# Optimization experiments

Measured on AMD Instinct MI355X. Metric: run time of the kernel, lower is better.

Reference implementation:

```python
import jax, jax.numpy as jnp
import numpy as np

B, S, E, H, D = 4, 2048, 1024, 16, 64

def setup_inputs() -> dict:
    key = jax.random.key(0)
    ks = jax.random.split(key, 9)
    sc = 0.02
    return {
        "x":  jax.random.normal(ks[0], (B, S, E), jnp.float32),
        "Wq": jax.random.normal(ks[1], (H, E, D), jnp.float32) * sc,
        "bq": jax.random.normal(ks[2], (H, D), jnp.float32) * sc,
        "Wk": jax.random.normal(ks[3], (H, E, D), jnp.float32) * sc,
        "bk": jax.random.normal(ks[4], (H, D), jnp.float32) * sc,
        "Wv": jax.random.normal(ks[5], (H, E, D), jnp.float32) * sc,
        "bv": jax.random.normal(ks[6], (H, D), jnp.float32) * sc,
        "Wp": jax.random.normal(ks[7], (H * D, E), jnp.float32) * sc,
        "bp": jax.random.normal(ks[8], (E,), jnp.float32) * sc,
    }

def reference(x, Wq, bq, Wk, bk, Wv, bv, Wp, bp):
    # Per-head projections (stacked): [B,S,E] x [H,E,D] -> [B,H,S,D]
    q = jnp.einsum('bse,hed->bhsd', x, Wq) + bq[None, :, None, :]
    k = jnp.einsum('bse,hed->bhsd', x, Wk) + bk[None, :, None, :]
    v = jnp.einsum('bse,hed->bhsd', x, Wv) + bv[None, :, None, :]
    # Scaled scores with causal mask: [B,H,S,S]
    scores = jnp.einsum('bhqd,bhkd->bhqk', q, k) / jnp.sqrt(jnp.float32(D))
    causal = jnp.tril(jnp.ones((S, S), dtype=bool))
    scores = jnp.where(causal[None, None], scores, -jnp.inf)
    attn = jax.nn.softmax(scores, axis=-1)
    out = jnp.einsum('bhqk,bhkd->bhqd', attn, v)          # [B,H,S,D]
    out = out.transpose(0, 2, 1, 3).reshape(B, S, H * D)  # concat heads
    return out @ Wp + bp                                   # [B,S,E]
```

## Files before the change

kernel.cpp:

```cpp
#include <hip/hip_runtime.h>
#include <hip/hip_bf16.h>

#define B_ 4
#define S_ 2048
#define E_ 1024
#define H_ 16
#define D_ 64
#define QSCALE 0.18033688011112042f

typedef __attribute__((ext_vector_type(8))) short bf16x8;
typedef __attribute__((ext_vector_type(4))) float f32x4;

__device__ __forceinline__ f32x4 mfma16(bf16x8 a, bf16x8 b, f32x4 c) {
    return __builtin_amdgcn_mfma_f32_16x16x32_bf16(a, b, c, 0, 0, 0);
}
__device__ __forceinline__ short f2bs(float f) {
    __hip_bfloat16 h = __float2bfloat16(f);
    return *reinterpret_cast<short*>(&h);
}

__global__ __launch_bounds__(256) void conv_wqkv(
    const float* __restrict__ Wq, const float* __restrict__ Wk,
    const float* __restrict__ Wv, short* __restrict__ WT)
{
    const int mat = blockIdx.x >> 4;
    const int kt  = blockIdx.x & 15;
    const int which = mat >> 4, h = mat & 15;
    const float* src = (which == 0 ? Wq : which == 1 ? Wk : Wv) + (size_t)h * E_ * D_;
    __shared__ float T[64][65];
    const int tid = threadIdx.x;
    const int k0 = kt * 64;
    #pragma unroll
    for (int it = 0; it < 4; ++it) {
        int lin = tid + it * 256;
        int kr = lin >> 4, dc = (lin & 15) * 4;
        const float4 v = *(const float4*)&src[(size_t)(k0 + kr) * D_ + dc];
        T[kr][dc] = v.x; T[kr][dc + 1] = v.y; T[kr][dc + 2] = v.z; T[kr][dc + 3] = v.w;
    }
    __syncthreads();
    #pragma unroll
    for (int it = 0; it < 4; ++it) {
        int lin = tid + it * 256;
        int dr = lin >> 4, kc = (lin & 15) * 4;
        ushort4 o;
        o.x = (unsigned short)f2bs(T[kc][dr]);
        o.y = (unsigned short)f2bs(T[kc + 1][dr]);
        o.z = (unsigned short)f2bs(T[kc + 2][dr]);
        o.w = (unsigned short)f2bs(T[kc + 3][dr]);
        *(ushort4*)&WT[((size_t)mat * 64 + dr) * E_ + k0 + kc] = o;
    }
}

__global__ __launch_bounds__(256) void conv_wp(
    const float* __restrict__ Wp, short* __restrict__ WpT)
{
    const int ktile = blockIdx.x & 15, ntile = blockIdx.x >> 4;
    const int k0 = ktile * 64, n0 = ntile * 64;
    __shared__ float T[64][65];
    const int tid = threadIdx.x;
    #pragma unroll
    for (int it = 0; it < 4; ++it) {
        int lin = tid + it * 256;
        int kr = lin >> 4, nc = (lin & 15) * 4;
        const float4 v = *(const float4*)&Wp[(size_t)(k0 + kr) * E_ + n0 + nc];
        T[kr][nc] = v.x; T[kr][nc + 1] = v.y; T[kr][nc + 2] = v.z; T[kr][nc + 3] = v.w;
    }
    __syncthreads();
    #pragma unroll
    for (int it = 0; it < 4; ++it) {
        int lin = tid + it * 256;
        int nr = lin >> 4, kc = (lin & 15) * 4;
        ushort4 o;
        o.x = (unsigned short)f2bs(T[kc][nr]);
        o.y = (unsigned short)f2bs(T[kc + 1][nr]);
        o.z = (unsigned short)f2bs(T[kc + 2][nr]);
        o.w = (unsigned short)f2bs(T[kc + 3][nr]);
        *(ushort4*)&WpT[(size_t)(n0 + nr) * E_ + k0 + kc] = o;
    }
}

__global__ __launch_bounds__(256, 2) void qkv_fused(
    const float* __restrict__ x, const short* __restrict__ WT,
    const float* __restrict__ bq, const float* __restrict__ bk,
    const float* __restrict__ bv,
    short* __restrict__ Qw, short* __restrict__ Kw, short* __restrict__ VTw)
{
    const int h = blockIdx.y;
    const int m0 = blockIdx.x * 128;
    __shared__ short Xs[128 * 72];
    __shared__ short Wt3[3][64 * 72];

    const int tid = threadIdx.x;
    const int lane = tid & 63, w = tid >> 6;
    const int l15 = lane & 15, qd = lane >> 4;

    f32x4 zero = {0.f, 0.f, 0.f, 0.f};
    f32x4 acc[3][2][4];
    #pragma unroll
    for (int a = 0; a < 3; ++a)
        #pragma unroll
        for (int b = 0; b < 2; ++b)
            #pragma unroll
            for (int c = 0; c < 4; ++c) acc[a][b][c] = zero;

    float4 xr[4][2];
    bf16x8 wr[6];

    #pragma unroll
    for (int it = 0; it < 4; ++it) {
        int lin = tid + it * 256;
        int row = lin >> 3, cb = (lin & 7) * 8;
        xr[it][0] = *(const float4*)&x[(size_t)(m0 + row) * E_ + cb];
        xr[it][1] = *(const float4*)&x[(size_t)(m0 + row) * E_ + cb + 4];
    }
    #pragma unroll
    for (int it = 0; it < 6; ++it) {
        int lin = tid + it * 256;
        int mat = lin >> 9, rem = lin & 511;
        int d = rem >> 3, cb = (rem & 7) * 8;
        wr[it] = *(const bf16x8*)&WT[((size_t)(mat * 16 + h) * 64 + d) * E_ + cb];
    }

    for (int k0 = 0; k0 < E_; k0 += 64) {
        #pragma unroll
        for (int it = 0; it < 4; ++it) {
            int lin = tid + it * 256;
            int row = lin >> 3, cb = (lin & 7) * 8;
            bf16x8 pk;
            pk[0] = f2bs(xr[it][0].x); pk[1] = f2bs(xr[it][0].y);
            pk[2] = f2bs(xr[it][0].z); pk[3] = f2bs(xr[it][0].w);
            pk[4] = f2bs(xr[it][1].x); pk[5] = f2bs(xr[it][1].y);
            pk[6] = f2bs(xr[it][1].z); pk[7] = f2bs(xr[it][1].w);
            *(bf16x8*)&Xs[row * 72 + cb] = pk;
        }
        #pragma unroll
        for (int it = 0; it < 6; ++it) {
            int lin = tid + it * 256;
            int mat = lin >> 9, rem = lin & 511;
            int d = rem >> 3, cb = (rem & 7) * 8;
            *(bf16x8*)&Wt3[mat][d * 72 + cb] = wr[it];
        }
        __syncthreads();
        if (k0 + 64 < E_) {
            #pragma unroll
            for (int it = 0; it < 4; ++it) {
                int lin = tid + it * 256;
                int row = lin >> 3, cb = (lin & 7) * 8;
                xr[it][0] = *(const float4*)&x[(size_t)(m0 + row) * E_ + k0 + 64 + cb];
                xr[it][1] = *(const float4*)&x[(size_t)(m0 + row) * E_ + k0 + 64 + cb + 4];
            }
            #pragma unroll
            for (int it = 0; it < 6; ++it) {
                int lin = tid + it * 256;
                int mat = lin >> 9, rem = lin & 511;
                int d = rem >> 3, cb = (rem & 7) * 8;
                wr[it] = *(const bf16x8*)&WT[((size_t)(mat * 16 + h) * 64 + d) * E_ + k0 + 64 + cb];
            }
        }
        #pragma unroll
        for (int t = 0; t < 2; ++t) {
            bf16x8 am0 = *(const bf16x8*)&Xs[(w * 32 + l15) * 72 + t * 32 + qd * 8];
            bf16x8 am1 = *(const bf16x8*)&Xs[(w * 32 + 16 + l15) * 72 + t * 32 + qd * 8];
            #pragma unroll
            for (int mat = 0; mat < 3; ++mat)
                #pragma unroll
                for (int c = 0; c < 4; ++c) {
                    bf16x8 bb = *(const bf16x8*)&Wt3[mat][(c * 16 + l15) * 72 + t * 32 + qd * 8];
                    acc[mat][0][c] = mfma16(am0, bb, acc[mat][0][c]);
                    acc[mat][1][c] = mfma16(am1, bb, acc[mat][1][c]);
                }
        }
        __syncthreads();
    }

    const int bb = m0 >> 11;
    const int s0 = m0 & (S_ - 1);
    float bqv[4], bkv[4], bvv[4];
    #pragma unroll
    for (int c = 0; c < 4; ++c) {
        int d = c * 16 + l15;
        bqv[c] = bq[h * D_ + d];
        bkv[c] = bk[h * D_ + d];
        bvv[c] = bv[h * D_ + d];
    }
    #pragma unroll
    for (int mi = 0; mi < 2; ++mi)
        #pragma unroll
        for (int c = 0; c < 4; ++c)
            #pragma unroll
            for (int r = 0; r < 4; ++r) {
                int s = s0 + w * 32 + mi * 16 + qd * 4 + r;
                size_t base = (((size_t)bb * H_ + h) * S_ + s) * D_ + c * 16 + l15;
                Qw[base] = f2bs((acc[0][mi][c][r] + bqv[c]) * QSCALE);
                Kw[base] = f2bs(acc[1][mi][c][r] + bkv[c]);
            }
    short* ep = Xs + w * (32 * 66);
    #pragma unroll
    for (int mi = 0; mi < 2; ++mi)
        #pragma unroll
        for (int c = 0; c < 4; ++c)
            #pragma unroll
            for (int r = 0; r < 4; ++r)
                ep[(mi * 16 + qd * 4 + r) * 66 + c * 16 + l15] =
                    f2bs(acc[2][mi][c][r] + bvv[c]);
    asm volatile("s_waitcnt lgkmcnt(0)" ::: "memory");
    const int sr = lane & 31, dh = lane >> 5;
    const size_t vbase = ((size_t)bb * H_ + h) * (size_t)D_ * S_;
    #pragma unroll
    for (int it = 0; it < 32; ++it) {
        int dd = it * 2 + dh;
        VTw[vbase + (size_t)dd * S_ + s0 + w * 32 + sr] = ep[sr * 66 + dd];
    }
}

__global__ __launch_bounds__(256, 2) void attn(
    const short* __restrict__ Qw, const short* __restrict__ Kw,
    const short* __restrict__ VTw, short* __restrict__ Ow)
{
    const int jj = blockIdx.x;
    const int bh = blockIdx.y;
    const int b = bh >> 4, h = bh & 15;
    const size_t kbase = ((size_t)b * H_ + h) * (size_t)S_ * D_;
    const size_t vbase = ((size_t)b * H_ + h) * (size_t)D_ * S_;

    __shared__ short Qs[128 * 72];
    __shared__ short Ks[2][64 * 72];
    __shared__ short Vt[2][64 * 72];

    const int tid = threadIdx.x;
    const int lane = tid & 63, w = tid >> 6;
    const int l15 = lane & 15, qd = lane >> 4;

    const int r0s = tid >> 3;
    const int c0s = (tid & 7) * 8;
    const int r1s = r0s + 32;

    #pragma unroll
    for (int phase = 0; phase < 2; ++phase) {
        const int qt = phase ? jj : (15 - jj);

        #pragma unroll
        for (int it = 0; it < 4; ++it) {
            int row = w * 32 + it * 8 + (lane >> 3);
            int cb = (lane & 7) * 8;
            *(bf16x8*)&Qs[row * 72 + cb] =
                *(const bf16x8*)&Qw[kbase + (size_t)(qt * 128 + row) * D_ + cb];
        }
        asm volatile("s_waitcnt lgkmcnt(0)" ::: "memory");
        bf16x8 qf[2][2];
        #pragma unroll
        for (int mi = 0; mi < 2; ++mi)
            #pragma unroll
            for (int t = 0; t < 2; ++t)
                qf[mi][t] = *(const bf16x8*)&Qs[(w * 32 + mi * 16 + l15) * 72 + t * 32 + qd * 8];

        f32x4 zero = {0.f, 0.f, 0.f, 0.f};
        f32x4 oacc[2][4];
        float lrow[2][4];
        #pragma unroll
        for (int mi = 0; mi < 2; ++mi) {
            #pragma unroll
            for (int c = 0; c < 4; ++c) oacc[mi][c] = zero;
            #pragma unroll
            for (int r = 0; r < 4; ++r) lrow[mi][r] = 0.f;
        }

        const int nkt = (qt + 1) * 2;
        bf16x8 kr0, kr1, vr0, vr1;
        kr0 = *(const bf16x8*)&Kw[kbase + (size_t)r0s * D_ + c0s];
        kr1 = *(const bf16x8*)&Kw[kbase + (size_t)r1s * D_ + c0s];
        vr0 = *(const bf16x8*)&VTw[vbase + (size_t)r0s * S_ + c0s];
        vr1 = *(const bf16x8*)&VTw[vbase + (size_t)r1s * S_ + c0s];
        *(bf16x8*)&Ks[0][r0s * 72 + c0s] = kr0;
        *(bf16x8*)&Ks[0][r1s * 72 + c0s] = kr1;
        *(bf16x8*)&Vt[0][r0s * 72 + c0s] = vr0;
        *(bf16x8*)&Vt[0][r1s * 72 + c0s] = vr1;
        __syncthreads();

        int p = 0;
        for (int kt = 0; kt < nkt; ++kt) {
            const bool pre = (kt + 1 < nkt);
            if (pre) {
                kr0 = *(const bf16x8*)&Kw[kbase + (size_t)((kt + 1) * 64 + r0s) * D_ + c0s];
                kr1 = *(const bf16x8*)&Kw[kbase + (size_t)((kt + 1) * 64 + r1s) * D_ + c0s];
                vr0 = *(const bf16x8*)&VTw[vbase + (size_t)r0s * S_ + (kt + 1) * 64 + c0s];
                vr1 = *(const bf16x8*)&VTw[vbase + (size_t)r1s * S_ + (kt + 1) * 64 + c0s];
            }
            f32x4 sc[2][4];
            #pragma unroll
            for (int mi = 0; mi < 2; ++mi)
                #pragma unroll
                for (int c = 0; c < 4; ++c) sc[mi][c] = zero;
            #pragma unroll
            for (int t = 0; t < 2; ++t)
                #pragma unroll
                for (int c = 0; c < 4; ++c) {
                    bf16x8 bk = *(const bf16x8*)&Ks[p][(c * 16 + l15) * 72 + t * 32 + qd * 8];
                    sc[0][c] = mfma16(qf[0][t], bk, sc[0][c]);
                    sc[1][c] = mfma16(qf[1][t], bk, sc[1][c]);
                }
            #pragma unroll
            for (int mi = 0; mi < 2; ++mi) {
                const int fr = qt * 128 + w * 32 + mi * 16;
                if (kt * 64 + 63 > fr) {
                    #pragma unroll
                    for (int c = 0; c < 4; ++c) {
                        int col = kt * 64 + c * 16 + l15;
                        #pragma unroll
                        for (int r = 0; r < 4; ++r)
                            if (col > fr + qd * 4 + r) sc[mi][c][r] = -1e30f;
                    }
                }
                #pragma unroll
                for (int c = 0; c < 4; ++c)
                    #pragma unroll
                    for (int r = 0; r < 4; ++r) {
                        float pv = __builtin_amdgcn_exp2f(sc[mi][c][r]);
                        lrow[mi][r] += pv;
                        Qs[(w * 32 + mi * 16 + qd * 4 + r) * 72 + c * 16 + l15] = f2bs(pv);
                    }
            }
            asm volatile("s_waitcnt lgkmcnt(0)" ::: "memory");
            #pragma unroll
            for (int t = 0; t < 2; ++t) {
                bf16x8 ap0 = *(const bf16x8*)&Qs[(w * 32 + l15) * 72 + t * 32 + qd * 8];
                bf16x8 ap1 = *(const bf16x8*)&Qs[(w * 32 + 16 + l15) * 72 + t * 32 + qd * 8];
                #pragma unroll
                for (int c = 0; c < 4; ++c) {
                    bf16x8 bv = *(const bf16x8*)&Vt[p][(c * 16 + l15) * 72 + t * 32 + qd * 8];
                    oacc[0][c] = mfma16(ap0, bv, oacc[0][c]);
                    oacc[1][c] = mfma16(ap1, bv, oacc[1][c]);
                }
            }
            if (pre) {
                *(bf16x8*)&Ks[1 - p][r0s * 72 + c0s] = kr0;
                *(bf16x8*)&Ks[1 - p][r1s * 72 + c0s] = kr1;
                *(bf16x8*)&Vt[1 - p][r0s * 72 + c0s] = vr0;
                *(bf16x8*)&Vt[1 - p][r1s * 72 + c0s] = vr1;
            }
            __syncthreads();
            p ^= 1;
        }

        #pragma unroll
        for (int mi = 0; mi < 2; ++mi) {
            float inv[4];
            #pragma unroll
            for (int r = 0; r < 4; ++r) {
                float l = lrow[mi][r];
                l += __shfl_xor(l, 1);
                l += __shfl_xor(l, 2);
                l += __shfl_xor(l, 4);
                l += __shfl_xor(l, 8);
                inv[r] = 1.f / l;
            }
            #pragma unroll
            for (int c = 0; c < 4; ++c)
                #pragma unroll
                for (int r = 0; r < 4; ++r) {
                    int s = qt * 128 + w * 32 + mi * 16 + qd * 4 + r;
                    Ow[((size_t)b * S_ + s) * (H_ * D_) + h * D_ + c * 16 + l15] =
                        f2bs(oacc[mi][c][r] * inv[r]);
                }
        }
    }
}

__global__ __launch_bounds__(256, 3) void out_proj(
    const short* __restrict__ Oin, const short* __restrict__ WpT,
    const float* __restrict__ bp, float* __restrict__ out)
{
    const int m0 = blockIdx.x * 128;
    const int n0 = blockIdx.y * 64;
    __shared__ short As[128 * 72];
    __shared__ short Bs[64 * 72];
    const int tid = threadIdx.x;
    const int lane = tid & 63, w = tid >> 6;
    const int l15 = lane & 15, qd = lane >> 4;

    f32x4 zero = {0.f, 0.f, 0.f, 0.f};
    f32x4 acc[2][4];
    #pragma unroll
    for (int mi = 0; mi < 2; ++mi)
        #pragma unroll
        for (int c = 0; c < 4; ++c) acc[mi][c] = zero;

    bf16x8 ar[4], br[2];
    #pragma unroll
    for (int it = 0; it < 4; ++it) {
        int lin = tid + it * 256;
        int row = lin >> 3, cb = (lin & 7) * 8;
        ar[it] = *(const bf16x8*)&Oin[(size_t)(m0 + row) * E_ + cb];
    }
    #pragma unroll
    for (int it = 0; it < 2; ++it) {
        int lin = tid + it * 256;
        int row = lin >> 3, cb = (lin & 7) * 8;
        br[it] = *(const bf16x8*)&WpT[(size_t)(n0 + row) * E_ + cb];
    }

    for (int k0 = 0; k0 < E_; k0 += 64) {
        #pragma unroll
        for (int it = 0; it < 4; ++it) {
            int lin = tid + it * 256;
            int row = lin >> 3, cb = (lin & 7) * 8;
            *(bf16x8*)&As[row * 72 + cb] = ar[it];
        }
        #pragma unroll
        for (int it = 0; it < 2; ++it) {
            int lin = tid + it * 256;
            int row = lin >> 3, cb = (lin & 7) * 8;
            *(bf16x8*)&Bs[row * 72 + cb] = br[it];
        }
        __syncthreads();
        if (k0 + 64 < E_) {
            #pragma unroll
            for (int it = 0; it < 4; ++it) {
                int lin = tid + it * 256;
                int row = lin >> 3, cb = (lin & 7) * 8;
                ar[it] = *(const bf16x8*)&Oin[(size_t)(m0 + row) * E_ + k0 + 64 + cb];
            }
            #pragma unroll
            for (int it = 0; it < 2; ++it) {
                int lin = tid + it * 256;
                int row = lin >> 3, cb = (lin & 7) * 8;
                br[it] = *(const bf16x8*)&WpT[(size_t)(n0 + row) * E_ + k0 + 64 + cb];
            }
        }
        #pragma unroll
        for (int t = 0; t < 2; ++t) {
            bf16x8 a0 = *(const bf16x8*)&As[(w * 32 + l15) * 72 + t * 32 + qd * 8];
            bf16x8 a1 = *(const bf16x8*)&As[(w * 32 + 16 + l15) * 72 + t * 32 + qd * 8];
            #pragma unroll
            for (int c = 0; c < 4; ++c) {
                bf16x8 bb = *(const bf16x8*)&Bs[(c * 16 + l15) * 72 + t * 32 + qd * 8];
                acc[0][c] = mfma16(a0, bb, acc[0][c]);
                acc[1][c] = mfma16(a1, bb, acc[1][c]);
            }
        }
        __syncthreads();
    }
    #pragma unroll
    for (int mi = 0; mi < 2; ++mi)
        #pragma unroll
        for (int c = 0; c < 4; ++c) {
            float bpv = bp[n0 + c * 16 + l15];
            #pragma unroll
            for (int r = 0; r < 4; ++r) {
                int m = m0 + w * 32 + mi * 16 + qd * 4 + r;
                out[(size_t)m * E_ + n0 + c * 16 + l15] = acc[mi][c][r] + bpv;
            }
        }
}

extern "C" void kernel_launch(void* const* d_in, const int* in_sizes, int n_in,
                              void* d_out, int out_size, void* d_ws, size_t ws_size,
                              hipStream_t stream)
{
    const float* x  = (const float*)d_in[0];
    const float* Wq = (const float*)d_in[1];
    const float* bq = (const float*)d_in[2];
    const float* Wk = (const float*)d_in[3];
    const float* bk = (const float*)d_in[4];
    const float* Wv = (const float*)d_in[5];
    const float* bv = (const float*)d_in[6];
    const float* Wp = (const float*)d_in[7];
    const float* bp = (const float*)d_in[8];
    float* out = (float*)d_out;

    const size_t nQKV = (size_t)B_ * H_ * S_ * D_;
    short* Qw   = (short*)d_ws;
    short* Kw   = Qw + nQKV;
    short* VTw  = Kw + nQKV;
    short* buf3 = VTw + nQKV;
    short* WT   = buf3;
    short* Ow   = buf3;
    short* WpT  = Qw;

    conv_wqkv<<<dim3(768), 256, 0, stream>>>(Wq, Wk, Wv, WT);
    qkv_fused<<<dim3(64, 16), 256, 0, stream>>>(x, WT, bq, bk, bv, Qw, Kw, VTw);
    attn<<<dim3(8, 64), 256, 0, stream>>>(Qw, Kw, VTw, Ow);
    conv_wp<<<dim3(256), 256, 0, stream>>>(Wp, WpT);
    out_proj<<<dim3(64, 16), 256, 0, stream>>>(Ow, WpT, bp, out);
}
```

Baseline: 261.4 us.

## Switch QKV and output projections to 32x32 MFMA with k-slab LDS layout

Both projection GEMMs now use 32x32x16 bf16 MFMA with a 2x2 wave grid instead of 16x16x32 tiles, and shared memory is reorganized into per-k-chunk slabs (padded strides) to cut LDS read traffic and bank conflicts. The output projection tile grows to 128x128 (grid halved), raising arithmetic intensity but lowering occupancy. The V transpose epilogue now goes through a shared buffer with 16-byte vectorized global stores. Register pressure rises from the larger f32x16 accumulators.

Result: faster. 252.3 us (-3.5%).

```diff
diff --git a/kernel.cpp b/kernel.cpp
--- a/kernel.cpp
+++ b/kernel.cpp
@@ -10,14 +10,21 @@
 
 typedef __attribute__((ext_vector_type(8))) short bf16x8;
 typedef __attribute__((ext_vector_type(4))) float f32x4;
+typedef __attribute__((ext_vector_type(16))) float f32x16;
 
 __device__ __forceinline__ f32x4 mfma16(bf16x8 a, bf16x8 b, f32x4 c) {
     return __builtin_amdgcn_mfma_f32_16x16x32_bf16(a, b, c, 0, 0, 0);
+}
+__device__ __forceinline__ f32x16 mfma32(bf16x8 a, bf16x8 b, f32x16 c) {
+    return __builtin_amdgcn_mfma_f32_32x32x16_bf16(a, b, c, 0, 0, 0);
 }
 __device__ __forceinline__ short f2bs(float f) {
     __hip_bfloat16 h = __float2bfloat16(f);
     return *reinterpret_cast<short*>(&h);
 }
+
+#define XSLAB 1032
+#define WSLAB 1544
 
 __global__ __launch_bounds__(256) void conv_wqkv(
     const float* __restrict__ Wq, const float* __restrict__ Wk,
@@ -87,129 +94,128 @@
 {
     const int h = blockIdx.y;
     const int m0 = blockIdx.x * 128;
-    __shared__ short Xs[128 * 72];
-    __shared__ short Wt3[3][64 * 72];
+    __shared__ short SM[8 * XSLAB + 8 * WSLAB];
+    short* Xs = SM;
+    short* Ws = SM + 8 * XSLAB;
 
     const int tid = threadIdx.x;
     const int lane = tid & 63, w = tid >> 6;
-    const int l15 = lane & 15, qd = lane >> 4;
-
-    f32x4 zero = {0.f, 0.f, 0.f, 0.f};
-    f32x4 acc[3][2][4];
-    #pragma unroll
-    for (int a = 0; a < 3; ++a)
-        #pragma unroll
-        for (int b = 0; b < 2; ++b)
-            #pragma unroll
-            for (int c = 0; c < 4; ++c) acc[a][b][c] = zero;
+    const int wm = w & 1, wn = w >> 1;
+    const int l31 = lane & 31, hi = lane >> 5;
+    const int cc = tid & 7, r8 = tid >> 3;
+
+    f32x16 acc[2][3];
+    #pragma unroll
+    for (int mf = 0; mf < 2; ++mf)
+        #pragma unroll
+        for (int nf = 0; nf < 3; ++nf)
+            #pragma unroll
+            for (int i = 0; i < 16; ++i) acc[mf][nf][i] = 0.f;
 
     float4 xr[4][2];
     bf16x8 wr[6];
 
     #pragma unroll
     for (int it = 0; it < 4; ++it) {
-        int lin = tid + it * 256;
-        int row = lin >> 3, cb = (lin & 7) * 8;
-        xr[it][0] = *(const float4*)&x[(size_t)(m0 + row) * E_ + cb];
-        xr[it][1] = *(const float4*)&x[(size_t)(m0 + row) * E_ + cb + 4];
+        const float* p = &x[(size_t)(m0 + it * 32 + r8) * E_ + cc * 8];
+        xr[it][0] = *(const float4*)p;
+        xr[it][1] = *(const float4*)(p + 4);
     }
     #pragma unroll
     for (int it = 0; it < 6; ++it) {
-        int lin = tid + it * 256;
-        int mat = lin >> 9, rem = lin & 511;
-        int d = rem >> 3, cb = (rem & 7) * 8;
-        wr[it] = *(const bf16x8*)&WT[((size_t)(mat * 16 + h) * 64 + d) * E_ + cb];
+        int rg = ((it >> 1) * 16 + h) * 64 + (it & 1) * 32 + r8;
+        wr[it] = *(const bf16x8*)&WT[(size_t)rg * E_ + cc * 8];
     }
 
     for (int k0 = 0; k0 < E_; k0 += 64) {
         #pragma unroll
         for (int it = 0; it < 4; ++it) {
-            int lin = tid + it * 256;
-            int row = lin >> 3, cb = (lin & 7) * 8;
             bf16x8 pk;
             pk[0] = f2bs(xr[it][0].x); pk[1] = f2bs(xr[it][0].y);
             pk[2] = f2bs(xr[it][0].z); pk[3] = f2bs(xr[it][0].w);
             pk[4] = f2bs(xr[it][1].x); pk[5] = f2bs(xr[it][1].y);
             pk[6] = f2bs(xr[it][1].z); pk[7] = f2bs(xr[it][1].w);
-            *(bf16x8*)&Xs[row * 72 + cb] = pk;
-        }
-        #pragma unroll
-        for (int it = 0; it < 6; ++it) {
-            int lin = tid + it * 256;
-            int mat = lin >> 9, rem = lin & 511;
-            int d = rem >> 3, cb = (rem & 7) * 8;
-            *(bf16x8*)&Wt3[mat][d * 72 + cb] = wr[it];
-        }
+            *(bf16x8*)&Xs[cc * XSLAB + (it * 32 + r8) * 8] = pk;
+        }
+        #pragma unroll
+        for (int it = 0; it < 6; ++it)
+            *(bf16x8*)&Ws[cc * WSLAB + (it * 32 + r8) * 8] = wr[it];
         __syncthreads();
         if (k0 + 64 < E_) {
             #pragma unroll
             for (int it = 0; it < 4; ++it) {
-                int lin = tid + it * 256;
-                int row = lin >> 3, cb = (lin & 7) * 8;
-                xr[it][0] = *(const float4*)&x[(size_t)(m0 + row) * E_ + k0 + 64 + cb];
-                xr[it][1] = *(const float4*)&x[(size_t)(m0 + row) * E_ + k0 + 64 + cb + 4];
+                const float* p = &x[(size_t)(m0 + it * 32 + r8) * E_ + k0 + 64 + cc * 8];
+                xr[it][0] = *(const float4*)p;
+                xr[it][1] = *(const float4*)(p + 4);
             }
             #pragma unroll
             for (int it = 0; it < 6; ++it) {
-                int lin = tid + it * 256;
-                int mat = lin >> 9, rem = lin & 511;
-                int d = rem >> 3, cb = (rem & 7) * 8;
-                wr[it] = *(const bf16x8*)&WT[((size_t)(mat * 16 + h) * 64 + d) * E_ + k0 + 64 + cb];
-            }
-        }
-        #pragma unroll
-        for (int t = 0; t < 2; ++t) {
-            bf16x8 am0 = *(const bf16x8*)&Xs[(w * 32 + l15) * 72 + t * 32 + qd * 8];
-            bf16x8 am1 = *(const bf16x8*)&Xs[(w * 32 + 16 + l15) * 72 + t * 32 + qd * 8];
-            #pragma unroll
-            for (int mat = 0; mat < 3; ++mat)
-                #pragma unroll
-                for (int c = 0; c < 4; ++c) {
-                    bf16x8 bb = *(const bf16x8*)&Wt3[mat][(c * 16 + l15) * 72 + t * 32 + qd * 8];
-                    acc[mat][0][c] = mfma16(am0, bb, acc[mat][0][c]);
-                    acc[mat][1][c] = mfma16(am1, bb, acc[mat][1][c]);
-                }
+                int rg = ((it >> 1) * 16 + h) * 64 + (it & 1) * 32 + r8;
+                wr[it] = *(const bf16x8*)&WT[(size_t)rg * E_ + k0 + 64 + cc * 8];
+            }
+        }
+        #pragma unroll
+        for (int ks = 0; ks < 4; ++ks) {
+            const int ccr = ks * 2 + hi;
+            bf16x8 a[2], b[3];
+            #pragma unroll
+            for (int mf = 0; mf < 2; ++mf)
+                a[mf] = *(const bf16x8*)&Xs[ccr * XSLAB + (wm * 64 + mf * 32 + l31) * 8];
+            #pragma unroll
+            for (int nf = 0; nf < 3; ++nf)
+                b[nf] = *(const bf16x8*)&Ws[ccr * WSLAB + (wn * 96 + nf * 32 + l31) * 8];
+            #pragma unroll
+            for (int mf = 0; mf < 2; ++mf)
+                #pragma unroll
+                for (int nf = 0; nf < 3; ++nf)
+                    acc[mf][nf] = mfma32(a[mf], b[nf], acc[mf][nf]);
         }
         __syncthreads();
     }
 
     const int bb = m0 >> 11;
     const int s0 = m0 & (S_ - 1);
-    float bqv[4], bkv[4], bvv[4];
-    #pragma unroll
-    for (int c = 0; c < 4; ++c) {
-        int d = c * 16 + l15;
-        bqv[c] = bq[h * D_ + d];
-        bkv[c] = bk[h * D_ + d];
-        bvv[c] = bv[h * D_ + d];
-    }
-    #pragma unroll
-    for (int mi = 0; mi < 2; ++mi)
-        #pragma unroll
-        for (int c = 0; c < 4; ++c)
-            #pragma unroll
-            for (int r = 0; r < 4; ++r) {
-                int s = s0 + w * 32 + mi * 16 + qd * 4 + r;
-                size_t base = (((size_t)bb * H_ + h) * S_ + s) * D_ + c * 16 + l15;
-                Qw[base] = f2bs((acc[0][mi][c][r] + bqv[c]) * QSCALE);
-                Kw[base] = f2bs(acc[1][mi][c][r] + bkv[c]);
-            }
-    short* ep = Xs + w * (32 * 66);
-    #pragma unroll
-    for (int mi = 0; mi < 2; ++mi)
-        #pragma unroll
-        for (int c = 0; c < 4; ++c)
-            #pragma unroll
-            for (int r = 0; r < 4; ++r)
-                ep[(mi * 16 + qd * 4 + r) * 66 + c * 16 + l15] =
-                    f2bs(acc[2][mi][c][r] + bvv[c]);
-    asm volatile("s_waitcnt lgkmcnt(0)" ::: "memory");
-    const int sr = lane & 31, dh = lane >> 5;
+    const size_t qkbase = ((size_t)bb * H_ + h) * S_;
+    short* Vr = SM;
+    #pragma unroll
+    for (int mf = 0; mf < 2; ++mf)
+        #pragma unroll
+        for (int nf = 0; nf < 3; ++nf) {
+            const int ng = wn * 96 + nf * 32;
+            const int mat = ng >> 6;
+            const int d = (ng & 63) + l31;
+            const int sl0 = wm * 64 + mf * 32 + 4 * hi;
+            if (mat == 0) {
+                const float bb_ = bq[h * D_ + d];
+                #pragma unroll
+                for (int rg = 0; rg < 16; ++rg) {
+                    int s = s0 + sl0 + (rg & 3) + 8 * (rg >> 2);
+                    Qw[(qkbase + s) * D_ + d] = f2bs((acc[mf][nf][rg] + bb_) * QSCALE);
+                }
+            } else if (mat == 1) {
+                const float bb_ = bk[h * D_ + d];
+                #pragma unroll
+                for (int rg = 0; rg < 16; ++rg) {
+                    int s = s0 + sl0 + (rg & 3) + 8 * (rg >> 2);
+                    Kw[(qkbase + s) * D_ + d] = f2bs(acc[mf][nf][rg] + bb_);
+                }
+            } else {
+                const float bb_ = bv[h * D_ + d];
+                #pragma unroll
+                for (int rg = 0; rg < 16; ++rg) {
+                    int sl = sl0 + (rg & 3) + 8 * (rg >> 2);
+                    Vr[d * 136 + sl] = f2bs(acc[mf][nf][rg] + bb_);
+                }
+            }
+        }
+    __syncthreads();
     const size_t vbase = ((size_t)bb * H_ + h) * (size_t)D_ * S_;
-    #pragma unroll
-    for (int it = 0; it < 32; ++it) {
-        int dd = it * 2 + dh;
-        VTw[vbase + (size_t)dd * S_ + s0 + w * 32 + sr] = ep[sr * 66 + dd];
+    const int sc = tid & 15, dr = tid >> 4;
+    #pragma unroll
+    for (int it = 0; it < 4; ++it) {
+        int d = it * 16 + dr;
+        *(bf16x8*)&VTw[vbase + (size_t)d * S_ + s0 + sc * 8] =
+            *(const bf16x8*)&Vr[d * 136 + sc * 8];
     }
 }
 
@@ -366,89 +372,80 @@
     }
 }
 
-__global__ __launch_bounds__(256, 3) void out_proj(
+__global__ __launch_bounds__(256, 2) void out_proj(
     const short* __restrict__ Oin, const short* __restrict__ WpT,
     const float* __restrict__ bp, float* __restrict__ out)
 {
     const int m0 = blockIdx.x * 128;
-    const int n0 = blockIdx.y * 64;
-    __shared__ short As[128 * 72];
-    __shared__ short Bs[64 * 72];
+    const int n0 = blockIdx.y * 128;
+    __shared__ short SM2[16 * XSLAB];
+    short* As = SM2;
+    short* Bs = SM2 + 8 * XSLAB;
+
     const int tid = threadIdx.x;
     const int lane = tid & 63, w = tid >> 6;
-    const int l15 = lane & 15, qd = lane >> 4;
-
-    f32x4 zero = {0.f, 0.f, 0.f, 0.f};
-    f32x4 acc[2][4];
-    #pragma unroll
-    for (int mi = 0; mi < 2; ++mi)
-        #pragma unroll
-        for (int c = 0; c < 4; ++c) acc[mi][c] = zero;
-
-    bf16x8 ar[4], br[2];
-    #pragma unroll
-    for (int it = 0; it < 4; ++it) {
-        int lin = tid + it * 256;
-        int row = lin >> 3, cb = (lin & 7) * 8;
-        ar[it] = *(const bf16x8*)&Oin[(size_t)(m0 + row) * E_ + cb];
-    }
-    #pragma unroll
-    for (int it = 0; it < 2; ++it) {
-        int lin = tid + it * 256;
-        int row = lin >> 3, cb = (lin & 7) * 8;
-        br[it] = *(const bf16x8*)&WpT[(size_t)(n0 + row) * E_ + cb];
+    const int wm = w & 1, wn = w >> 1;
+    const int l31 = lane & 31, hi = lane >> 5;
+    const int cc = tid & 7, r8 = tid >> 3;
+
+    f32x16 acc[2][2];
+    #pragma unroll
+    for (int mf = 0; mf < 2; ++mf)
+        #pragma unroll
+        for (int nf = 0; nf < 2; ++nf)
+            #pragma unroll
+            for (int i = 0; i < 16; ++i) acc[mf][nf][i] = 0.f;
+
+    bf16x8 ar[4], br[4];
+    #pragma unroll
+    for (int it = 0; it < 4; ++it) {
+        ar[it] = *(const bf16x8*)&Oin[(size_t)(m0 + it * 32 + r8) * E_ + cc * 8];
+        br[it] = *(const bf16x8*)&WpT[(size_t)(n0 + it * 32 + r8) * E_ + cc * 8];
     }
 
     for (int k0 = 0; k0 < E_; k0 += 64) {
         #pragma unroll
         for (int it = 0; it < 4; ++it) {
-            int lin = tid + it * 256;
-            int row = lin >> 3, cb = (lin & 7) * 8;
-            *(bf16x8*)&As[row * 72 + cb] = ar[it];
-        }
-        #pragma unroll
-        for (int it = 0; it < 2; ++it) {
-            int lin = tid + it * 256;
-            int row = lin >> 3, cb = (lin & 7) * 8;
-            *(bf16x8*)&Bs[row * 72 + cb] = br[it];
+            *(bf16x8*)&As[cc * XSLAB + (it * 32 + r8) * 8] = ar[it];
+            *(bf16x8*)&Bs[cc * XSLAB + (it * 32 + r8) * 8] = br[it];
         }
         __syncthreads();
         if (k0 + 64 < E_) {
             #pragma unroll
             for (int it = 0; it < 4; ++it) {
-                int lin = tid + it * 256;
-                int row = lin >> 3, cb = (lin & 7) * 8;
-                ar[it] = *(const bf16x8*)&Oin[(size_t)(m0 + row) * E_ + k0 + 64 + cb];
-            }
-            #pragma unroll
-            for (int it = 0; it < 2; ++it) {
-                int lin = tid + it * 256;
-                int row = lin >> 3, cb = (lin & 7) * 8;
-                br[it] = *(const bf16x8*)&WpT[(size_t)(n0 + row) * E_ + k0 + 64 + cb];
-            }
-        }
-        #pragma unroll
-        for (int t = 0; t < 2; ++t) {
-            bf16x8 a0 = *(const bf16x8*)&As[(w * 32 + l15) * 72 + t * 32 + qd * 8];
-            bf16x8 a1 = *(const bf16x8*)&As[(w * 32 + 16 + l15) * 72 + t * 32 + qd * 8];
-            #pragma unroll
-            for (int c = 0; c < 4; ++c) {
-                bf16x8 bb = *(const bf16x8*)&Bs[(c * 16 + l15) * 72 + t * 32 + qd * 8];
-                acc[0][c] = mfma16(a0, bb, acc[0][c]);
-                acc[1][c] = mfma16(a1, bb, acc[1][c]);
-            }
+                ar[it] = *(const bf16x8*)&Oin[(size_t)(m0 + it * 32 + r8) * E_ + k0 + 64 + cc * 8];
+                br[it] = *(const bf16x8*)&WpT[(size_t)(n0 + it * 32 + r8) * E_ + k0 + 64 + cc * 8];
+            }
+        }
+        #pragma unroll
+        for (int ks = 0; ks < 4; ++ks) {
+            const int ccr = ks * 2 + hi;
+            bf16x8 a[2], b[2];
+            #pragma unroll
+            for (int mf = 0; mf < 2; ++mf)
+                a[mf] = *(const bf16x8*)&As[ccr * XSLAB + (wm * 64 + mf * 32 + l31) * 8];
+            #pragma unroll
+            for (int nf = 0; nf < 2; ++nf)
+                b[nf] = *(const bf16x8*)&Bs[ccr * XSLAB + (wn * 64 + nf * 32 + l31) * 8];
+            #pragma unroll
+            for (int mf = 0; mf < 2; ++mf)
+                #pragma unroll
+                for (int nf = 0; nf < 2; ++nf)
+                    acc[mf][nf] = mfma32(a[mf], b[nf], acc[mf][nf]);
         }
         __syncthreads();
     }
     #pragma unroll
-    for (int mi = 0; mi < 2; ++mi)
-        #pragma unroll
-        for (int c = 0; c < 4; ++c) {
-            float bpv = bp[n0 + c * 16 + l15];
-            #pragma unroll
-            for (int r = 0; r < 4; ++r) {
-                int m = m0 + w * 32 + mi * 16 + qd * 4 + r;
-                out[(size_t)m * E_ + n0 + c * 16 + l15] = acc[mi][c][r] + bpv;
+    for (int mf = 0; mf < 2; ++mf)
+        #pragma unroll
+        for (int nf = 0; nf < 2; ++nf) {
+            const int n = n0 + wn * 64 + nf * 32 + l31;
+            const float bpv = bp[n];
+            const int sl0 = wm * 64 + mf * 32 + 4 * hi;
+            #pragma unroll
+            for (int rg = 0; rg < 16; ++rg) {
+                int m = m0 + sl0 + (rg & 3) + 8 * (rg >> 2);
+                out[(size_t)m * E_ + n] = acc[mf][nf][rg] + bpv;
             }
         }
 }
@@ -481,5 +478,5 @@
     qkv_fused<<<dim3(64, 16), 256, 0, stream>>>(x, WT, bq, bk, bv, Qw, Kw, VTw);
     attn<<<dim3(8, 64), 256, 0, stream>>>(Qw, Kw, VTw, Ow);
     conv_wp<<<dim3(256), 256, 0, stream>>>(Wp, WpT);
-    out_proj<<<dim3(64, 16), 256, 0, stream>>>(Ow, WpT, bp, out);
-}
+    out_proj<<<dim3(64, 8), 256, 0, stream>>>(Ow, WpT, bp, out);
+}
```
